# Optimization experiments

Hardware: AMD Instinct MI355X
Metric: run time of the kernel (lower is better)

Reference implementation:

```python
import jax, jax.numpy as jnp
import numpy as np
import math

B, S, D = 4, 2048, 768
H = 12
DH = D // H  # 64


def setup_inputs() -> dict:
    key = jax.random.key(0)
    ks = jax.random.split(key, 10)
    sc = 1.0 / math.sqrt(D)
    x = jax.random.normal(ks[0], (B, S, D), dtype=jnp.float32)
    # per-head QKV weights stacked: [H, D, DH]; biases [H, DH]
    Wq = jax.random.normal(ks[1], (H, D, DH), dtype=jnp.float32) * sc
    bq = jnp.zeros((H, DH), dtype=jnp.float32)
    Wk = jax.random.normal(ks[2], (H, D, DH), dtype=jnp.float32) * sc
    bk = jnp.zeros((H, DH), dtype=jnp.float32)
    Wv = jax.random.normal(ks[3], (H, D, DH), dtype=jnp.float32) * sc
    bv = jnp.zeros((H, DH), dtype=jnp.float32)
    # output projection: maps concat(all_head) [H*DH] -> D
    Wo = jax.random.normal(ks[4], (H * DH, D), dtype=jnp.float32) * sc
    bo = jnp.zeros((D,), dtype=jnp.float32)
    return {"x": x, "Wq": Wq, "bq": bq, "Wk": Wk, "bk": bk,
            "Wv": Wv, "bv": bv, "Wo": Wo, "bo": bo}


def reference(x, Wq, bq, Wk, bk, Wv, bv, Wo, bo):
    # Batched over heads: equivalent to the per-head Python loop in the original.
    q = jnp.einsum('bnd,hde->bhne', x, Wq) + bq[None, :, None, :]
    k = jnp.einsum('bnd,hde->bhne', x, Wk) + bk[None, :, None, :]
    v = jnp.einsum('bnd,hde->bhne', x, Wv) + bv[None, :, None, :]
    scores = jnp.einsum('bhne,bhme->bhnm', q, k) / jnp.sqrt(jnp.asarray(DH, x.dtype))
    probs = jax.nn.softmax(scores, axis=-1)  # [B,H,S,S] dominant intermediate
    ctx = jnp.einsum('bhnm,bhme->bhne', probs, v)  # [B,H,S,DH]
    # concat heads along feature dim -> [B,S,H*DH]
    ctx = jnp.transpose(ctx, (0, 2, 1, 3)).reshape(x.shape[0], x.shape[1], H * DH)
    out = ctx @ Wo + bo
    return out
```

## Files before the change

### kernel.cpp

```cpp
#include <hip/hip_runtime.h>
#include <hip/hip_bf16.h>
#include <stdint.h>

typedef __bf16 bf16;
typedef bf16 bf16x8 __attribute__((ext_vector_type(8)));
typedef bf16 bf16x4 __attribute__((ext_vector_type(4)));
typedef float f32x4 __attribute__((ext_vector_type(4)));

#define B_   4
#define S_   2048
#define D_   768
#define H_   12
#define DH_  64
#define M_   (B_ * S_)

#define QSCALE (0.125f * 1.44269504088896f)
#define SM_SHIFT 12.0f

#define MFMA32(a, b, c) __builtin_amdgcn_mfma_f32_16x16x32_bf16(a, b, c, 0, 0, 0)

#if __has_builtin(__builtin_amdgcn_exp2f)
#define EXP2(x) __builtin_amdgcn_exp2f(x)
#else
#define EXP2(x) exp2f(x)
#endif

__device__ __forceinline__ float scrub(float v) { return (v == v) ? v : 0.0f; }

__device__ __forceinline__ bf16x4 pack4(float p0, float p1, float p2, float p3) {
    union { uint32_t u[2]; bf16x4 v; } o;
    uint32_t a0 = __builtin_bit_cast(uint32_t, p0) + 0x8000u;
    uint32_t a1 = __builtin_bit_cast(uint32_t, p1) + 0x8000u;
    uint32_t a2 = __builtin_bit_cast(uint32_t, p2) + 0x8000u;
    uint32_t a3 = __builtin_bit_cast(uint32_t, p3) + 0x8000u;
    o.u[0] = __builtin_amdgcn_perm(a1, a0, 0x07060302u);
    o.u[1] = __builtin_amdgcn_perm(a3, a2, 0x07060302u);
    return o.v;
}

__device__ __forceinline__ int swz(int row, int col8) {
    return row * 64 + ((col8 ^ (row & 7)) << 3);
}
__device__ __forceinline__ int swzK(int row, int col8) {
    return row * 64 + (((col8 ^ (row & 7) ^ (((row >> 3) & 1) << 2))) << 3);
}

__device__ __forceinline__ int xcd_remap(int lid, int nwg_div8) {
    return (lid & 7) * nwg_div8 + (lid >> 3);
}

#if __has_builtin(__builtin_amdgcn_global_load_lds)
#define ASYNC_STAGE 1
#endif
__device__ __forceinline__ void stage16(bf16* ldsbase, const bf16* g) {
#ifdef ASYNC_STAGE
    __builtin_amdgcn_global_load_lds(
        (const __attribute__((address_space(1))) void*)g,
        (__attribute__((address_space(3))) void*)ldsbase, 16, 0, 0);
#else
    int l = threadIdx.x & 63;
    *(uint4*)(ldsbase + l * 8) = *(const uint4*)g;
#endif
}

__global__ void prep(const void* __restrict__ x,
                     const void* __restrict__ Wq, const void* __restrict__ Wk,
                     const void* __restrict__ Wv, const void* __restrict__ Wo,
                     const void* __restrict__ bq, const void* __restrict__ bk,
                     const void* __restrict__ bv, const void* __restrict__ bo,
                     bf16* __restrict__ Xb, bf16* __restrict__ WTc,
                     bf16* __restrict__ WoT, float* __restrict__ biasC,
                     float* __restrict__ boF, int* __restrict__ flg)
{
    __shared__ int cnt[4];
    __shared__ int isb_sh;
    __shared__ float T[64][65];
    const int tid = threadIdx.x;
    {
        const uint32_t* xw = (const uint32_t*)x;
        int c = 0;
        for (int i = tid * 16; i < tid * 16 + 16; i++) {
            uint32_t e = (xw[i] >> 7) & 0xFFu;
            c += (e >= 100u && e <= 150u) ? 1 : 0;
        }
        #pragma unroll
        for (int off = 32; off; off >>= 1) c += __shfl_xor(c, off, 64);
        if ((tid & 63) == 0) cnt[tid >> 6] = c;
    }
    __syncthreads();
    if (tid == 0) {
        int t = cnt[0] + cnt[1] + cnt[2] + cnt[3];
        isb_sh = (t > 2458) ? 1 : 0;
        if (blockIdx.x == 0) flg[0] = isb_sh;
    }
    __syncthreads();
    const int isb = isb_sh;
    const int blk = blockIdx.x;

    if (blk < 3072) {
        int i = (blk * 256 + tid) * 8;
        if (isb) {
            *(uint4*)(Xb + i) = *(const uint4*)((const bf16*)x + i);
        } else {
            const float4* s = (const float4*)((const float*)x + i);
            float4 f0 = s[0], f1 = s[1];
            bf16x8 v;
            v[0] = (bf16)f0.x; v[1] = (bf16)f0.y; v[2] = (bf16)f0.z; v[3] = (bf16)f0.w;
            v[4] = (bf16)f1.x; v[5] = (bf16)f1.y; v[6] = (bf16)f1.z; v[7] = (bf16)f1.w;
            *(bf16x8*)(Xb + i) = v;
        }
    } else if (blk < 3648) {
        int g = blk - 3072;
        int dt = g % 12, hn = (g / 12) % 12, z = g / 144;
        const void* src = (z == 0) ? Wq : (z == 1) ? Wk : (z == 2) ? Wv : Wo;
        {
            int row = tid >> 2, c = (tid & 3) * 16;
            size_t sbase = (z < 3) ? ((size_t)hn * D_ + dt * 64 + row) * 64 + c
                                   : ((size_t)(dt * 64 + row)) * D_ + hn * 64 + c;
            if (isb) { const bf16* s = (const bf16*)src + sbase;
                #pragma unroll
                for (int j = 0; j < 16; j++) T[row][c + j] = (float)s[j];
            } else { const float* s = (const float*)src + sbase;
                #pragma unroll
                for (int j = 0; j < 16; j++) T[row][c + j] = s[j];
            }
        }
        __syncthreads();
        {
            int rr = tid >> 2, cc = (tid & 3) * 16;
            bf16x8 v0, v1;
            #pragma unroll
            for (int j = 0; j < 8; j++) { v0[j] = (bf16)T[cc + j][rr]; v1[j] = (bf16)T[cc + 8 + j][rr]; }
            bf16* dst = (z < 3) ? WTc : WoT;
            size_t dbase = (z < 3) ? ((size_t)(z * D_ + hn * 64 + rr)) * D_ + dt * 64 + cc
                                   : ((size_t)(hn * 64 + rr)) * D_ + dt * 64 + cc;
            *(bf16x8*)(dst + dbase) = v0;
            *(bf16x8*)(dst + dbase + 8) = v1;
        }
    } else {
        int i = (blk - 3648) * 256 + tid;
        if (i < 3072) {
            const void* src; float* dst; int j, di;
            if (i < 2304) { int p = i / 768; j = i - p * 768;
                src = (p == 0) ? bq : (p == 1) ? bk : bv; dst = biasC; di = i; }
            else { src = bo; j = i - 2304; dst = boF; di = j; }
            dst[di] = isb ? (float)((const bf16*)src)[j] : ((const float*)src)[j];
        }
    }
}

template<int MODE>
__global__ __launch_bounds__(256) void gemm128(
    const bf16* __restrict__ A, const bf16* __restrict__ BT,
    const float* __restrict__ bias,
    bf16* __restrict__ Qo, bf16* __restrict__ Ko, bf16* __restrict__ Vt,
    void* __restrict__ out, const int* __restrict__ flagp)
{
    constexpr int BN = (MODE == 0) ? 128 : 64;
    constexpr int NI = (MODE == 0) ? 4 : 2;
    __shared__ bf16 smem[2 * 128 * 64 + 2 * BN * 64];

    const int mt = blockIdx.x, nt = blockIdx.y;
    const int tid = threadIdx.x, lane = tid & 63, w = tid >> 6;
    const int quad = lane >> 4, ln = lane & 15;
    const int wm = w & 1, wn = w >> 1;

    f32x4 acc[4][NI] = {};
    const int rl = lane >> 3;
    const int cb = (lane & 7) ^ rl;

    const bf16* Ap = A  + (size_t)(mt * 128 + rl) * D_ + cb * 8;
    const bf16* Bp = BT + (size_t)(nt * BN + rl) * D_ + cb * 8;

    auto gstage = [&](int buf, const bf16* ap, const bf16* bp) {
        bf16* al = smem + buf * (128 * 64);
        bf16* bl = smem + 2 * 128 * 64 + buf * (BN * 64);
        #pragma unroll
        for (int j = 0; j < 4; j++)
            stage16(al + (w * 32 + j * 8) * 64, ap + (size_t)(w * 32 + j * 8) * D_);
        #pragma unroll
        for (int j = 0; j < BN / 32; j++)
            stage16(bl + (w * (BN / 4) + j * 8) * 64, bp + (size_t)(w * (BN / 4) + j * 8) * D_);
    };

    gstage(0, Ap, Bp);
    int cur = 0;
    for (int ks = 0; ks < D_; ks += 64) {
        __syncthreads();
        Ap += 64; Bp += 64;
        if (ks + 64 < D_) gstage(cur ^ 1, Ap, Bp);
        const bf16* Ac = smem + cur * (128 * 64);
        const bf16* Bc = smem + 2 * 128 * 64 + cur * (BN * 64);
        #pragma unroll
        for (int kc = 0; kc < 2; kc++) {
            bf16x8 a[4], b[NI];
            #pragma unroll
            for (int i = 0; i < 4; i++)
                a[i] = *(const bf16x8*)(Ac + swz(wm * 64 + i * 16 + ln, (kc << 2) | quad));
            #pragma unroll
            for (int i = 0; i < NI; i++)
                b[i] = *(const bf16x8*)(Bc + swz(wn * (BN / 2) + i * 16 + ln, (kc << 2) | quad));
            #pragma unroll
            for (int mi = 0; mi < 4; mi++)
                #pragma unroll
                for (int ni = 0; ni < NI; ni++)
                    acc[mi][ni] = MFMA32(a[mi], b[ni], acc[mi][ni]);
        }
        cur ^= 1;
    }

    if constexpr (MODE == 0) {
        const int nbase = nt * 128 + wn * 64;
        if (nt < 12) {
            const int proj = nbase / 768;
            const float scale = (proj == 0) ? QSCALE : 1.0f;
            bf16* dst = (proj == 0) ? Qo : Ko;
            __syncthreads();
            bf16* epi = smem;
            #pragma unroll
            for (int ni = 0; ni < 4; ni++) {
                int e = ni * 16 + ln;
                float bb = bias[nbase + e];
                #pragma unroll
                for (int mi = 0; mi < 4; mi++)
                    #pragma unroll
                    for (int r = 0; r < 4; r++) {
                        int mrow = wm * 64 + mi * 16 + quad * 4 + r;
                        epi[mrow * 136 + wn * 64 + e] =
                            (bf16)scrub((acc[mi][ni][r] + bb) * scale);
                    }
            }
            __syncthreads();
            const int bi = (mt * 128) >> 11, s0 = (mt * 128) & (S_ - 1);
            const int nh0 = ((nt * 128) % 768) >> 6;
            #pragma unroll
            for (int pass = 0; pass < 8; pass++) {
                int mrow = pass * 16 + (tid >> 4);
                int col = (tid & 15) * 8;
                uint4 v = *(const uint4*)(epi + mrow * 136 + col);
                int head = col >> 6, e = col & 63;
                *(uint4*)(dst + ((size_t)(bi * H_ + nh0 + head) * S_ + s0 + mrow) * 64 + e) = v;
            }
        } else {
            __syncthreads();
            bf16* epi = smem;
            #pragma unroll
            for (int ni = 0; ni < 4; ni++) {
                float bb = bias[nbase + ni * 16 + ln];
                int row = wn * 64 + ni * 16 + ln;
                #pragma unroll
                for (int mi = 0; mi < 4; mi++)
                    #pragma unroll
                    for (int r = 0; r < 4; r++) {
                        int scol = wm * 64 + mi * 16 + quad * 4 + r;
                        epi[row * 136 + scol] = (bf16)scrub(acc[mi][ni][r] + bb);
                    }
            }
            __syncthreads();
            const int bi = (mt * 128) >> 11, s0 = (mt * 128) & (S_ - 1);
            const int nh0 = ((nt * 128) % 768) >> 6;
            #pragma unroll
            for (int pass = 0; pass < 8; pass++) {
                int row2 = pass * 16 + (tid >> 4);
                int sl = (tid & 15) * 8;
                uint4 v = *(const uint4*)(epi + row2 * 136 + sl);
                int head = row2 >> 6, e = row2 & 63;
                *(uint4*)(Vt + ((size_t)(bi * H_ + nh0 + head) * 64 + e) * S_ + s0 + sl) = v;
            }
        }
    } else {
        const int isb = flagp[0];
        __syncthreads();
        if (isb) {
            bf16* epi = smem;
            #pragma unroll
            for (int ni = 0; ni < NI; ni++) {
                int e = wn * 32 + ni * 16 + ln;
                float bb = bias[nt * 64 + e];
                #pragma unroll
                for (int mi = 0; mi < 4; mi++)
                    #pragma unroll
                    for (int r = 0; r < 4; r++) {
                        int mrow = wm * 64 + mi * 16 + quad * 4 + r;
                        epi[mrow * 72 + e] = (bf16)scrub(acc[mi][ni][r] + bb);
                    }
            }
            __syncthreads();
            #pragma unroll
            for (int pass = 0; pass < 4; pass++) {
                int mrow = pass * 32 + (tid >> 3);
                int col = (tid & 7) * 8;
                uint4 v = *(const uint4*)(epi + mrow * 72 + col);
                *(uint4*)((bf16*)out + (size_t)(mt * 128 + mrow) * D_ + nt * 64 + col) = v;
            }
        } else {
            float* epi = (float*)smem;
            #pragma unroll
            for (int ni = 0; ni < NI; ni++) {
                int e = wn * 32 + ni * 16 + ln;
                float bb = bias[nt * 64 + e];
                #pragma unroll
                for (int mi = 0; mi < 4; mi++)
                    #pragma unroll
                    for (int r = 0; r < 4; r++) {
                        int mrow = wm * 64 + mi * 16 + quad * 4 + r;
                        epi[mrow * 68 + e] = scrub(acc[mi][ni][r] + bb);
                    }
            }
            __syncthreads();
            #pragma unroll
            for (int pass = 0; pass < 8; pass++) {
                int mrow = pass * 16 + (tid >> 4);
                int col = (tid & 15) * 4;
                uint4 v = *(const uint4*)(epi + mrow * 68 + col);
                *(uint4*)((float*)out + (size_t)(mt * 128 + mrow) * D_ + nt * 64 + col) = v;
            }
        }
    }
}

__global__ __launch_bounds__(256)
__attribute__((amdgpu_waves_per_eu(3, 3)))
void attn(
    const bf16* __restrict__ Q, const bf16* __restrict__ K, const bf16* __restrict__ Vt,
    bf16* __restrict__ ctx)
{
    __shared__ bf16 Kl[2][64 * 64];
    __shared__ bf16 Vl[2][64 * 64];

    const int lid = blockIdx.y * 16 + blockIdx.x;
    const int sid = xcd_remap(lid, 96);
    const int qt = sid & 15, bh = sid >> 4;
    const int tid = threadIdx.x, lane = tid & 63, w = tid >> 6;
    const int quad = lane >> 4, ln = lane & 15;
    const size_t base = (size_t)bh * (S_ * 64);

    bf16x8 qf[2][2];
    #pragma unroll
    for (int s = 0; s < 2; s++) {
        int qrow = qt * 128 + w * 32 + s * 16 + ln;
        qf[s][0] = *(const bf16x8*)(Q + base + (size_t)qrow * 64 + quad * 8);
        qf[s][1] = *(const bf16x8*)(Q + base + (size_t)qrow * 64 + 32 + quad * 8);
    }

    const f32x4 cinit = {-SM_SHIFT, -SM_SHIFT, -SM_SHIFT, -SM_SHIFT};
    bf16x8 vone8;
    #pragma unroll
    for (int i = 0; i < 8; i++) vone8[i] = (bf16)1.0f;

    f32x4 acc[2][4] = {};
    f32x4 accl[2] = {};

    const int rl = lane >> 3;
    const int cbv = (lane & 7) ^ rl;
    const bf16* Kg = K  + base + (size_t)rl * 64;
    const bf16* Vg = Vt + base + (size_t)rl * S_ + cbv * 8;

    auto stageKV = [&](bf16* kl, bf16* vl, const bf16* kg, const bf16* vg) {
        #pragma unroll
        for (int j = 0; j < 2; j++) {
            int rbase = w * 16 + j * 8;
            int cbk = (lane & 7) ^ rl ^ ((j & 1) << 2);
            stage16(kl + rbase * 64, kg + (size_t)rbase * 64 + cbk * 8);
            stage16(vl + rbase * 64, vg + (size_t)rbase * S_);
        }
    };

    auto body = [&](const bf16* Kc, const bf16* Vc) {
        __builtin_amdgcn_s_setprio(1);
        #pragma unroll
        for (int p = 0; p < 2; p++) {
            bf16x8 k[2][2];
            #pragma unroll
            for (int t = 0; t < 2; t++) {
                int br = p * 32 + ((ln >> 2) << 3) + (t << 2) + (ln & 3);
                k[t][0] = *(const bf16x8*)(Kc + swzK(br, quad));
                k[t][1] = *(const bf16x8*)(Kc + swzK(br, 4 | quad));
            }
            bf16x8 vf[4];
            #pragma unroll
            for (int et = 0; et < 4; et++) {
                int vr = et * 16 + ln;
                vf[et] = *(const bf16x8*)(Vc + swz(vr, (p << 2) | quad));
            }
            #pragma unroll
            for (int s = 0; s < 2; s++) {
                f32x4 z0 = MFMA32(k[0][0], qf[s][0], cinit);
                z0 = MFMA32(k[0][1], qf[s][1], z0);
                f32x4 z1 = MFMA32(k[1][0], qf[s][0], cinit);
                z1 = MFMA32(k[1][1], qf[s][1], z1);
                union { bf16x4 h[2]; bf16x8 v; } pf;
                pf.h[0] = pack4(EXP2(z0[0]), EXP2(z0[1]), EXP2(z0[2]), EXP2(z0[3]));
                pf.h[1] = pack4(EXP2(z1[0]), EXP2(z1[1]), EXP2(z1[2]), EXP2(z1[3]));
                accl[s] = MFMA32(pf.v, vone8, accl[s]);
                #pragma unroll
                for (int et = 0; et < 4; et++)
                    acc[s][et] = MFMA32(pf.v, vf[et], acc[s][et]);
            }
        }
        __builtin_amdgcn_s_setprio(0);
    };

    stageKV(Kl[0], Vl[0], Kg, Vg);
    for (int kt = 0; kt < S_; kt += 128) {
        __syncthreads();
        stageKV(Kl[1], Vl[1], Kg + 64 * 64, Vg + 64);
        body(Kl[0], Vl[0]);
        __syncthreads();
        if (kt + 128 < S_) stageKV(Kl[0], Vl[0], Kg + 128 * 64, Vg + 128);
        body(Kl[1], Vl[1]);
        Kg += 128 * 64; Vg += 128;
    }

    const int bb = bh / H_, hh = bh - bb * H_;
    #pragma unroll
    for (int s = 0; s < 2; s++) {
        float linv[4];
        #pragma unroll
        for (int r = 0; r < 4; r++)
            linv[r] = 1.0f / accl[s][r];
        #pragma unroll
        for (int et = 0; et < 4; et++) {
            int e = et * 16 + ln;
            #pragma unroll
            for (int r = 0; r < 4; r++) {
                int srow_o = qt * 128 + w * 32 + s * 16 + quad * 4 + r;
                float v = scrub(acc[s][et][r] * linv[r]);
                ctx[((size_t)(bb * S_ + srow_o) * H_ + hh) * 64 + e] = (bf16)v;
            }
        }
    }
}

extern "C" void kernel_launch(void* const* d_in, const int* in_sizes, int n_in,
                              void* d_out, int out_size, void* d_ws, size_t ws_size,
                              hipStream_t stream) {
    const void* x  = d_in[0];
    const void* Wq = d_in[1];
    const void* bq = d_in[2];
    const void* Wk = d_in[3];
    const void* bk = d_in[4];
    const void* Wv = d_in[5];
    const void* bv = d_in[6];
    const void* Wo = d_in[7];
    const void* bo = d_in[8];

    char* ws = (char*)d_ws;
    bf16* Qb   = (bf16*)(ws);
    bf16* Kb   = (bf16*)(ws + 12582912);
    bf16* Vtb  = (bf16*)(ws + 25165824);
    bf16* Xb   = (bf16*)(ws + 37748736);
    bf16* Cb   = Xb;
    bf16* WTc  = (bf16*)(ws + 50331648);
    bf16* WoT  = (bf16*)(ws + 53870592);
    int*  flg  = (int*) (ws + 55050240);
    float* bC  = (float*)(ws + 55050496);
    float* boF = (float*)(ws + 55059712);
    (void)in_sizes; (void)n_in; (void)out_size; (void)ws_size;

    prep<<<3660, 256, 0, stream>>>(x, Wq, Wk, Wv, Wo, bq, bk, bv, bo,
                                   Xb, WTc, WoT, bC, boF, flg);

    gemm128<0><<<dim3(M_ / 128, 2304 / 128), 256, 0, stream>>>(
        Xb, WTc, bC, Qb, Kb, Vtb, nullptr, flg);

    attn<<<dim3(S_ / 128, B_ * H_), 256, 0, stream>>>(Qb, Kb, Vtb, Cb);

    gemm128<1><<<dim3(M_ / 128, D_ / 64), 256, 0, stream>>>(
        Cb, WoT, boF, nullptr, nullptr, nullptr, d_out, flg);
}
```

Before: 205.9 us.

## Split attention KV tile across wave pairs, each wave owning 64 query rows

Restructures the attention block so waves form pairs. Each wave holds 64 query rows instead of 32 and processes only half of each 64-key tile, rather than every wave sweeping all keys for its own 32 rows. This halves per-wave LDS reads of K/V fragments relative to MFMA work and batches the exp computations ahead of the PV MFMAs. The cost is doubled accumulator registers per wave (16 output accumulators plus 4 row sums), which raises register pressure under the fixed waves-per-EU constraint. It also adds a cross-wave reduction of partial outputs and row sums through LDS at the end, with extra syncthreads.

```diff
diff --git a/kernel.cpp b/kernel.cpp
--- a/kernel.cpp
+++ b/kernel.cpp
@@ -5,6 +5,7 @@
 typedef __bf16 bf16;
 typedef bf16 bf16x8 __attribute__((ext_vector_type(8)));
 typedef bf16 bf16x4 __attribute__((ext_vector_type(4)));
+typedef short s16x4 __attribute__((ext_vector_type(4)));
 typedef float f32x4 __attribute__((ext_vector_type(4)));
 
 #define B_   4
@@ -327,18 +328,20 @@
 {
     __shared__ bf16 Kl[2][64 * 64];
     __shared__ bf16 Vl[2][64 * 64];
+    __shared__ float sml[2][64];
 
     const int lid = blockIdx.y * 16 + blockIdx.x;
     const int sid = xcd_remap(lid, 96);
     const int qt = sid & 15, bh = sid >> 4;
     const int tid = threadIdx.x, lane = tid & 63, w = tid >> 6;
     const int quad = lane >> 4, ln = lane & 15;
+    const int wq = w >> 1, wm = w & 1;
     const size_t base = (size_t)bh * (S_ * 64);
 
-    bf16x8 qf[2][2];
+    bf16x8 qf[4][2];
     #pragma unroll
-    for (int s = 0; s < 2; s++) {
-        int qrow = qt * 128 + w * 32 + s * 16 + ln;
+    for (int s = 0; s < 4; s++) {
+        int qrow = qt * 128 + wq * 64 + s * 16 + ln;
         qf[s][0] = *(const bf16x8*)(Q + base + (size_t)qrow * 64 + quad * 8);
         qf[s][1] = *(const bf16x8*)(Q + base + (size_t)qrow * 64 + 32 + quad * 8);
     }
@@ -348,8 +351,8 @@
     #pragma unroll
     for (int i = 0; i < 8; i++) vone8[i] = (bf16)1.0f;
 
-    f32x4 acc[2][4] = {};
-    f32x4 accl[2] = {};
+    f32x4 acc[4][4] = {};
+    f32x4 accl[4] = {};
 
     const int rl = lane >> 3;
     const int cbv = (lane & 7) ^ rl;
@@ -368,35 +371,37 @@
 
     auto body = [&](const bf16* Kc, const bf16* Vc) {
         __builtin_amdgcn_s_setprio(1);
-        #pragma unroll
-        for (int p = 0; p < 2; p++) {
-            bf16x8 k[2][2];
-            #pragma unroll
-            for (int t = 0; t < 2; t++) {
-                int br = p * 32 + ((ln >> 2) << 3) + (t << 2) + (ln & 3);
-                k[t][0] = *(const bf16x8*)(Kc + swzK(br, quad));
-                k[t][1] = *(const bf16x8*)(Kc + swzK(br, 4 | quad));
-            }
-            bf16x8 vf[4];
-            #pragma unroll
-            for (int et = 0; et < 4; et++) {
-                int vr = et * 16 + ln;
-                vf[et] = *(const bf16x8*)(Vc + swz(vr, (p << 2) | quad));
-            }
-            #pragma unroll
-            for (int s = 0; s < 2; s++) {
-                f32x4 z0 = MFMA32(k[0][0], qf[s][0], cinit);
-                z0 = MFMA32(k[0][1], qf[s][1], z0);
-                f32x4 z1 = MFMA32(k[1][0], qf[s][0], cinit);
-                z1 = MFMA32(k[1][1], qf[s][1], z1);
-                union { bf16x4 h[2]; bf16x8 v; } pf;
-                pf.h[0] = pack4(EXP2(z0[0]), EXP2(z0[1]), EXP2(z0[2]), EXP2(z0[3]));
-                pf.h[1] = pack4(EXP2(z1[0]), EXP2(z1[1]), EXP2(z1[2]), EXP2(z1[3]));
-                accl[s] = MFMA32(pf.v, vone8, accl[s]);
-                #pragma unroll
-                for (int et = 0; et < 4; et++)
-                    acc[s][et] = MFMA32(pf.v, vf[et], acc[s][et]);
-            }
+        bf16x8 k[2][2];
+        #pragma unroll
+        for (int t = 0; t < 2; t++) {
+            int br = wm * 32 + ((ln >> 2) << 3) + (t << 2) + (ln & 3);
+            k[t][0] = *(const bf16x8*)(Kc + swzK(br, quad));
+            k[t][1] = *(const bf16x8*)(Kc + swzK(br, 4 | quad));
+        }
+        bf16x8 pf[4];
+        #pragma unroll
+        for (int s = 0; s < 4; s++) {
+            f32x4 z0 = MFMA32(k[0][0], qf[s][0], cinit);
+            z0 = MFMA32(k[0][1], qf[s][1], z0);
+            f32x4 z1 = MFMA32(k[1][0], qf[s][0], cinit);
+            z1 = MFMA32(k[1][1], qf[s][1], z1);
+            union { bf16x4 h[2]; bf16x8 v; } u;
+            u.h[0] = pack4(EXP2(z0[0]), EXP2(z0[1]), EXP2(z0[2]), EXP2(z0[3]));
+            u.h[1] = pack4(EXP2(z1[0]), EXP2(z1[1]), EXP2(z1[2]), EXP2(z1[3]));
+            pf[s] = u.v;
+        }
+        bf16x8 vf[4];
+        #pragma unroll
+        for (int et = 0; et < 4; et++) {
+            int vr = et * 16 + ln;
+            vf[et] = *(const bf16x8*)(Vc + swz(vr, (wm << 2) | quad));
+        }
+        #pragma unroll
+        for (int s = 0; s < 4; s++) {
+            accl[s] = MFMA32(pf[s], vone8, accl[s]);
+            #pragma unroll
+            for (int et = 0; et < 4; et++)
+                acc[s][et] = MFMA32(pf[s], vf[et], acc[s][et]);
         }
         __builtin_amdgcn_s_setprio(0);
     };
@@ -412,23 +417,36 @@
         Kg += 128 * 64; Vg += 128;
     }
 
-    const int bb = bh / H_, hh = bh - bb * H_;
-    #pragma unroll
-    for (int s = 0; s < 2; s++) {
-        float linv[4];
-        #pragma unroll
-        for (int r = 0; r < 4; r++)
-            linv[r] = 1.0f / accl[s][r];
-        #pragma unroll
-        for (int et = 0; et < 4; et++) {
-            int e = et * 16 + ln;
+    __syncthreads();
+    float* comb = wq ? (float*)Vl : (float*)Kl;
+    if (wm) {
+        #pragma unroll
+        for (int s = 0; s < 4; s++)
             #pragma unroll
             for (int r = 0; r < 4; r++) {
-                int srow_o = qt * 128 + w * 32 + s * 16 + quad * 4 + r;
-                float v = scrub(acc[s][et][r] * linv[r]);
-                ctx[((size_t)(bb * S_ + srow_o) * H_ + hh) * 64 + e] = (bf16)v;
-            }
-        }
+                int ql = s * 16 + quad * 4 + r;
+                if (ln == 0) sml[wq][ql] = accl[s][r];
+                #pragma unroll
+                for (int et = 0; et < 4; et++)
+                    comb[ql * 64 + et * 16 + ln] = acc[s][et][r];
+            }
+    }
+    __syncthreads();
+    if (!wm) {
+        const int bb = bh / H_, hh = bh - bb * H_;
+        #pragma unroll
+        for (int s = 0; s < 4; s++)
+            #pragma unroll
+            for (int r = 0; r < 4; r++) {
+                int ql = s * 16 + quad * 4 + r;
+                float linv = 1.0f / (accl[s][r] + sml[wq][ql]);
+                int srow_o = qt * 128 + wq * 64 + ql;
+                #pragma unroll
+                for (int et = 0; et < 4; et++) {
+                    float v = scrub((acc[s][et][r] + comb[ql * 64 + et * 16 + ln]) * linv);
+                    ctx[((size_t)(bb * S_ + srow_o) * H_ + hh) * 64 + et * 16 + ln] = (bf16)v;
+                }
+            }
     }
 }
 
```

Result: slower. 240.1 us (+16.6%).
